# Kernel tuning notes

Measured on AMD Instinct MI355X. Metric: run time of the kernel, lower is better.

The kernel has to match this reference:

```python
import jax, jax.numpy as jnp
import numpy as np

B, C, H, W = 4, 256, 64, 64

def _conv1x1(x, w, b):
    # x: [B,C,H,W], w: [O,C] (1x1 conv kernel squeezed), b: [O]
    return jnp.einsum('bchw,oc->bohw', x, w) + b[None, :, None, None]

def setup_inputs() -> dict:
    key = jax.random.key(0)
    ks = jax.random.split(key, 9)
    s = 1.0 / np.sqrt(C)
    inp = {'x': jax.random.normal(ks[0], (B, C, H, W), dtype=jnp.float32)}
    for i, name in enumerate(['f', 'g', 'h', 'v']):
        inp['W' + name] = jax.random.uniform(ks[1 + 2 * i], (C, C), jnp.float32, -s, s)
        inp['b' + name] = jax.random.uniform(ks[2 + 2 * i], (C,), jnp.float32, -s, s)
    return inp

def reference(x, Wf, bf, Wg, bg, Wh, bh, Wv, bv):
    b, c, h, w = x.shape
    n = h * w
    f = _conv1x1(x, Wf, bf).reshape(b, c, n)  # [B,C,N]
    g = _conv1x1(x, Wg, bg).reshape(b, c, n)  # [B,C,N]
    hh = _conv1x1(x, Wh, bh).reshape(b, c, n)  # [B,C,N]
    fg = jnp.einsum('bci,bcj->bij', f, g)      # [B,N,N], no scaling (as in source)
    attn = jax.nn.softmax(fg, axis=1)          # softmax over dim=1 (first N axis)
    fgh = jnp.einsum('bci,bij->bcj', hh, attn) # [B,C,N]
    return _conv1x1(fgh.reshape(b, c, h, w), Wv, bv)
```

## Files before the change

### kernel.cpp

```cpp
#include <hip/hip_runtime.h>
#include <hip/hip_bf16.h>


typedef short short8 __attribute__((ext_vector_type(8)));
typedef short short4v __attribute__((ext_vector_type(4)));
typedef float f32x4 __attribute__((ext_vector_type(4)));
typedef _Float16 f16x8 __attribute__((ext_vector_type(8)));
typedef unsigned short u16;
typedef unsigned int u32;

#define DEV static __device__ __forceinline__
#define MFMA16(a, b, c) __builtin_amdgcn_mfma_f32_16x16x32_f16(a, b, c, 0, 0, 0)

DEV u16 h16(float x) {
    union { _Float16 h; u16 u; } c;
    c.h = (_Float16)x;
    return c.u;
}
DEV f16x8 ldh8(const u16* p) { return *reinterpret_cast<const f16x8*>(p); }

DEV u32 cvtpk(float a, float b) {
    u32 r;
    asm("v_cvt_pkrtz_f16_f32 %0, %1, %2" : "=v"(r) : "v"(a), "v"(b));
    return r;
}

DEV void gload16(const void* g, void* l) {
    __builtin_amdgcn_global_load_lds(
        (const __attribute__((address_space(1))) unsigned int*)g,
        (__attribute__((address_space(3))) unsigned int*)l, 16, 0, 0);
}

constexpr size_t OFF_WH = 0;
constexpr size_t OFF_WV = 131072;
constexpr size_t OFF_MB = 262144;
constexpr size_t OFF_ML = 266240;
constexpr size_t OFF_M  = 524288;
constexpr size_t OFF_U  = 1310720;
constexpr size_t OFF_H  = OFF_U + 8388608;
constexpr size_t OFF_XT = OFF_H + 8388608;
constexpr size_t OFF_OP = OFF_XT + 8388608;

__global__ __launch_bounds__(256) void k_prep_w(
    const float* __restrict__ Wh, const float* __restrict__ Wv, u16* WH, u16* WV) {
    int i = blockIdx.x * 256 + threadIdx.x;
    WH[i] = h16(Wh[i]);
    WV[i] = h16(Wv[i]);
}

__global__ __launch_bounds__(256) void k_gemm_M(
    const float* __restrict__ Wf, const float* __restrict__ Wg,
    const float* __restrict__ bg, u16* __restrict__ M, float* __restrict__ Mb) {
    int c = blockIdx.x;
    int t = threadIdx.x;
    __shared__ float wf[256];
    wf[t] = Wf[(size_t)t * 256 + c];
    __syncthreads();
    float acc = 0.f;
    for (int o = 0; o < 256; ++o) acc += wf[o] * Wg[(size_t)o * 256 + t];
    M[(size_t)c * 256 + t] = h16(acc);
    if (t == 0) {
        float s = 0.f;
        for (int o = 0; o < 256; ++o) s += wf[o] * bg[o];
        Mb[c] = s;
    }
}

__global__ __launch_bounds__(256) void k_prep_x(const float* __restrict__ x, u16* Xt) {
    __shared__ float lds[64][65];
    int bid = blockIdx.x;
    int b = bid >> 8, rem = bid & 255, ct = rem >> 6, nt = rem & 63;
    int tid = threadIdx.x;
    int tx = tid & 63, ty = tid >> 6;
    const float* src = x + ((size_t)(b * 256 + ct * 64)) * 4096 + nt * 64;
#pragma unroll
    for (int k = 0; k < 16; ++k) {
        int cl = ty * 16 + k;
        lds[cl][tx] = src[(size_t)cl * 4096 + tx];
    }
    __syncthreads();
    int nl = tid >> 2, cg = tid & 3;
    short8 h0, h1;
#pragma unroll
    for (int j = 0; j < 8; ++j) h0[j] = (short)h16(lds[cg * 16 + j][nl]);
#pragma unroll
    for (int j = 8; j < 16; ++j) h1[j - 8] = (short)h16(lds[cg * 16 + j][nl]);
    size_t dst = ((size_t)(b * 4096 + nt * 64 + nl)) * 256 + ct * 64 + cg * 16;
    *reinterpret_cast<short8*>(Xt + dst) = h0;
    *reinterpret_cast<short8*>(Xt + dst + 8) = h1;
}

__global__ __launch_bounds__(256) void k_conv_u(
    const u16* __restrict__ Xt, const u16* __restrict__ M,
    const float* __restrict__ Mb, u16* U) {
    int bidm = blockIdx.x & 255, bido = blockIdx.x >> 8;
    int w = threadIdx.x >> 6, lane = threadIdx.x & 63, r = lane & 15, g = lane >> 4;
    int m0 = bidm * 64 + w * 16, o0 = bido * 64;
    f32x4 ua[4];
#pragma unroll
    for (int i = 0; i < 4; ++i) ua[i] = {0.f, 0.f, 0.f, 0.f};
    const u16* ar = Xt + (size_t)(m0 + r) * 256;
#pragma unroll
    for (int ks = 0; ks < 8; ++ks) {
        int k0 = ks * 32 + 8 * g;
        f16x8 a = ldh8(ar + k0);
#pragma unroll
        for (int ot = 0; ot < 4; ++ot) {
            size_t wrow = (size_t)(o0 + ot * 16 + r) * 256 + k0;
            ua[ot] = MFMA16(a, ldh8(M + wrow), ua[ot]);
        }
    }
#pragma unroll
    for (int ot = 0; ot < 4; ++ot) {
#pragma unroll
        for (int q = 0; q < 4; ++q) {
            int row = m0 + 4 * g + q;
            int col = o0 + ot * 16 + r;
            U[(size_t)row * 256 + col] = h16(ua[ot][q] + Mb[col]);
        }
    }
}

__global__ __launch_bounds__(256) void k_conv_h(
    const u16* __restrict__ WH, const u16* __restrict__ Xt,
    const float* __restrict__ bh, u16* Hb) {
    int bidn = blockIdx.x & 255, bido = blockIdx.x >> 8;
    int w = threadIdx.x >> 6, lane = threadIdx.x & 63, r = lane & 15, g = lane >> 4;
    int o0 = bido * 64 + w * 16, n0 = bidn * 64;
    f32x4 acc[4];
#pragma unroll
    for (int i = 0; i < 4; ++i) acc[i] = {0.f, 0.f, 0.f, 0.f};
    const u16* arow = WH + (size_t)(o0 + r) * 256;
#pragma unroll
    for (int ks = 0; ks < 8; ++ks) {
        int k0 = ks * 32 + 8 * g;
        f16x8 a = ldh8(arow + k0);
#pragma unroll
        for (int ntl = 0; ntl < 4; ++ntl) {
            f16x8 bb = ldh8(Xt + (size_t)(n0 + ntl * 16 + r) * 256 + k0);
            acc[ntl] = MFMA16(a, bb, acc[ntl]);
        }
    }
#pragma unroll
    for (int ntl = 0; ntl < 4; ++ntl) {
#pragma unroll
        for (int q = 0; q < 4; ++q) {
            int o = o0 + 4 * g + q;
            int nf = n0 + ntl * 16 + r;
            int bb = nf >> 12, n = nf & 4095;
            int k5 = n & 31;
            int kp = (k5 < 16) ? (8 * (k5 >> 2) + (k5 & 3))
                               : (8 * ((k5 - 16) >> 2) + 4 + (k5 & 3));
            int np = (n & ~31) | kp;
            Hb[((size_t)(bb * 256 + o)) * 4096 + np] = h16(acc[ntl][q] + bh[o]);
        }
    }
}

__global__ __launch_bounds__(256, 2) void k_attn(
    const u16* __restrict__ F, const u16* __restrict__ G,
    const u16* __restrict__ Hb, u16* __restrict__ OP, float* __restrict__ ML) {
    __shared__ u16 Kd[2][8192];
    __shared__ u16 Vd[2][8192];

    int bid = blockIdx.x;
    int xcd = bid & 7, idx = bid >> 3;
    int b = xcd >> 1, ks = xcd & 1;
    int tid = threadIdx.x;
    int w = tid >> 6, lane = tid & 63, r = lane & 15, g = lane >> 4;
    int j0 = idx * 64 + w * 16;
    const float L2E = 1.4426950408889634f;

    int vlc = (r >> 1) * 128 + (((16 * g) + (r & 1) * 64) ^ (((r >> 1) & 7) << 4));

    f16x8 Qf[8];
    {
        const u16* q = G + (size_t)(b * 4096 + j0 + r) * 256;
#pragma unroll
        for (int k = 0; k < 8; ++k) Qf[k] = ldh8(q + k * 32 + 8 * g);
    }
    f32x4 O[16];
#pragma unroll
    for (int i = 0; i < 16; ++i) O[i] = {0.f, 0.f, 0.f, 0.f};
    float m = -1e30f, l = 0.f;

    const char* Fb  = (const char*)(F + (size_t)b * 4096 * 256);
    const char* Hbb = (const char*)(Hb + (size_t)b * 256 * 4096);

    int ksrc[4], vsrc[4];
#pragma unroll
    for (int t = 0; t < 4; ++t) {
        int d = (w * 4 + t) * 1024 + lane * 16;
        int row = d >> 9, col = d & 511;
        ksrc[t] = row * 512 + (col ^ ((row & 7) << 4));
        int r128 = d >> 7, wn = d & 127;
        int wp = wn ^ ((r128 & 7) << 4);
        vsrc[t] = ((r128 * 2 + (wp >> 6)) << 13) + (wp & 63);
    }

#define STAGE(bufn, I0)                                                         \
    do {                                                                        \
        const char* kb_ = Fb + (size_t)(I0) * 512;                              \
        const char* vb_ = Hbb + (size_t)(I0) * 2;                               \
        char* kl = (char*)Kd[bufn];                                             \
        char* vl = (char*)Vd[bufn];                                             \
        _Pragma("unroll") for (int t = 0; t < 4; ++t)                           \
            gload16(kb_ + ksrc[t], kl + (w * 4 + t) * 1024);                    \
        _Pragma("unroll") for (int t = 0; t < 4; ++t)                           \
            gload16(vb_ + vsrc[t], vl + (w * 4 + t) * 1024);                    \
    } while (0)

    int i0beg = ks * 2048;
    STAGE(0, i0beg);
    __syncthreads();

    for (int it = 0; it < 64; ++it) {
        int cur = it & 1;
        if (it + 1 < 64) STAGE(cur ^ 1, i0beg + (it + 1) * 32);

        const char* Kl = (const char*)Kd[cur];
        const char* Vb = (const char*)Vd[cur] + vlc;

        f32x4 s0 = {0.f, 0.f, 0.f, 0.f};
        f32x4 s1 = {0.f, 0.f, 0.f, 0.f};
        __builtin_amdgcn_s_setprio(1);
        {
            const char* kr = Kl + r * 512;
            int sw = (r & 7) << 4;
#pragma unroll
            for (int k = 0; k < 8; ++k) {
                f16x8 ka = *reinterpret_cast<const f16x8*>(kr + ((k * 64 + 16 * g) ^ sw));
                s0 = MFMA16(ka, Qf[k], s0);
            }
        }
        {
            const char* kr = Kl + (16 + r) * 512;
            int sw = (r & 7) << 4;
#pragma unroll
            for (int k = 0; k < 8; ++k) {
                f16x8 ka = *reinterpret_cast<const f16x8*>(kr + ((k * 64 + 16 * g) ^ sw));
                s1 = MFMA16(ka, Qf[k], s1);
            }
        }
        __builtin_amdgcn_s_setprio(0);

        float v = fmaxf(fmaxf(fmaxf(s0[0], s0[1]), fmaxf(s0[2], s0[3])),
                        fmaxf(fmaxf(s1[0], s1[1]), fmaxf(s1[2], s1[3])));
        if (!__all(v - m <= 8.0f)) {
            v = fmaxf(v, __shfl_xor(v, 16));
            v = fmaxf(v, __shfl_xor(v, 32));
            float mn = fmaxf(m, v);
            float corr = exp2f((m - mn) * L2E);
            m = mn;
            l *= corr;
#pragma unroll
            for (int ct = 0; ct < 16; ++ct) O[ct] *= corr;
        }
#pragma unroll
        for (int q = 0; q < 4; ++q) {
            s0[q] = exp2f((s0[q] - m) * L2E);
            s1[q] = exp2f((s1[q] - m) * L2E);
        }
        l += (s0[0] + s0[1] + s0[2] + s0[3]) + (s1[0] + s1[1] + s1[2] + s1[3]);

        union { u32 wd[4]; f16x8 fr; } pu;
        pu.wd[0] = cvtpk(s0[0], s0[1]);
        pu.wd[1] = cvtpk(s0[2], s0[3]);
        pu.wd[2] = cvtpk(s1[0], s1[1]);
        pu.wd[3] = cvtpk(s1[2], s1[3]);

        __builtin_amdgcn_s_setprio(1);
#pragma unroll
        for (int ct = 0; ct < 16; ++ct) {
            f16x8 vb = *reinterpret_cast<const f16x8*>(Vb + ct * 1024);
            O[ct] = MFMA16(vb, pu.fr, O[ct]);
        }
        __builtin_amdgcn_s_setprio(0);

        __syncthreads();
    }
#undef STAGE

    l += __shfl_xor(l, 16);
    l += __shfl_xor(l, 32);
    float inv = 1.f / l;
    size_t mrow = (size_t)ks * 16384 + b * 4096 + j0 + r;
#pragma unroll
    for (int ct = 0; ct < 16; ++ct) {
        short4v pk;
#pragma unroll
        for (int q = 0; q < 4; ++q) pk[q] = (short)h16(O[ct][q] * inv);
        *reinterpret_cast<short4v*>(OP + mrow * 256 + ct * 16 + 4 * g) = pk;
    }
    if (g == 0) {
        size_t mi = mrow * 2;
        ML[mi] = m;
        ML[mi + 1] = l;
    }
}

__global__ __launch_bounds__(256) void k_conv_out(
    const u16* __restrict__ WV, const u16* __restrict__ OP,
    const float* __restrict__ ML, const float* __restrict__ bv,
    float* __restrict__ out) {
    int bidn = blockIdx.x & 255, bido = blockIdx.x >> 8;
    int w = threadIdx.x >> 6, lane = threadIdx.x & 63, r = lane & 15, g = lane >> 4;
    int o0 = bido * 64 + w * 16, n0 = bidn * 64;
    const float L2E = 1.4426950408889634f;
    float wl0[4], wl1[4];
    int nfs[4];
#pragma unroll
    for (int ntl = 0; ntl < 4; ++ntl) {
        int nf = n0 + ntl * 16 + r;
        nfs[ntl] = nf;
        float m0_ = ML[(size_t)nf * 2], l0_ = ML[(size_t)nf * 2 + 1];
        float m1_ = ML[((size_t)16384 + nf) * 2], l1_ = ML[((size_t)16384 + nf) * 2 + 1];
        float M_ = fmaxf(m0_, m1_);
        float a0 = exp2f((m0_ - M_) * L2E) * l0_;
        float a1 = exp2f((m1_ - M_) * L2E) * l1_;
        float inv = 1.f / (a0 + a1);
        wl0[ntl] = a0 * inv;
        wl1[ntl] = a1 * inv;
    }
    f32x4 acc[4];
#pragma unroll
    for (int i = 0; i < 4; ++i) acc[i] = {0.f, 0.f, 0.f, 0.f};
    const u16* arow = WV + (size_t)(o0 + r) * 256;
#pragma unroll
    for (int ks = 0; ks < 8; ++ks) {
        int k0 = ks * 32 + 8 * g;
        f16x8 a = ldh8(arow + k0);
#pragma unroll
        for (int ntl = 0; ntl < 4; ++ntl) {
            f16x8 v0 = ldh8(OP + (size_t)nfs[ntl] * 256 + k0);
            f16x8 v1 = ldh8(OP + ((size_t)16384 + nfs[ntl]) * 256 + k0);
            union { u32 wd[4]; f16x8 fr; } bb;
#pragma unroll
            for (int j = 0; j < 4; ++j) {
                float e0 = wl0[ntl] * (float)v0[2 * j] + wl1[ntl] * (float)v1[2 * j];
                float e1 = wl0[ntl] * (float)v0[2 * j + 1] + wl1[ntl] * (float)v1[2 * j + 1];
                bb.wd[j] = cvtpk(e0, e1);
            }
            acc[ntl] = MFMA16(a, bb.fr, acc[ntl]);
        }
    }
#pragma unroll
    for (int ntl = 0; ntl < 4; ++ntl) {
#pragma unroll
        for (int q = 0; q < 4; ++q) {
            int o = o0 + 4 * g + q;
            int nf = nfs[ntl];
            int bb2 = nf >> 12, n = nf & 4095;
            out[((size_t)(bb2 * 256 + o)) * 4096 + n] = acc[ntl][q] + bv[o];
        }
    }
}

extern "C" void kernel_launch(void* const* d_in, const int* in_sizes, int n_in,
                              void* d_out, int out_size, void* d_ws, size_t ws_size,
                              hipStream_t stream) {
    const float* x  = (const float*)d_in[0];
    const float* Wf = (const float*)d_in[1];
    const float* bf = (const float*)d_in[2];
    const float* Wg = (const float*)d_in[3];
    const float* bg = (const float*)d_in[4];
    const float* Wh = (const float*)d_in[5];
    const float* bh = (const float*)d_in[6];
    const float* Wv = (const float*)d_in[7];
    const float* bv = (const float*)d_in[8];
    float* out = (float*)d_out;
    char* ws = (char*)d_ws;
    (void)bf;

    u16* WH = (u16*)(ws + OFF_WH);
    u16* WV = (u16*)(ws + OFF_WV);
    float* MB = (float*)(ws + OFF_MB);
    float* ML = (float*)(ws + OFF_ML);
    u16* M  = (u16*)(ws + OFF_M);
    u16* U  = (u16*)(ws + OFF_U);
    u16* H  = (u16*)(ws + OFF_H);
    u16* XT = (u16*)(ws + OFF_XT);
    u16* OP = (u16*)(ws + OFF_OP);

    k_prep_w<<<256, 256, 0, stream>>>(Wh, Wv, WH, WV);
    k_gemm_M<<<256, 256, 0, stream>>>(Wf, Wg, bg, M, MB);
    k_prep_x<<<1024, 256, 0, stream>>>(x, XT);
    k_conv_u<<<1024, 256, 0, stream>>>(XT, M, MB, U);
    k_conv_h<<<1024, 256, 0, stream>>>(WH, XT, bh, H);
    k_attn<<<512, 256, 0, stream>>>(XT, U, H, OP, ML);
    k_conv_out<<<1024, 256, 0, stream>>>(WV, OP, ML, bv, out);
}
```

Before: 211.4 us.

## Fuse x transpose with U and H projections; fold weight cast into M kernel

The fp16 weight conversion moves into the M-product kernel. The x transpose, the U projection and the H projection merge into one kernel that keeps a 64-row x tile in LDS and reuses it for both GEMMs. This removes three launches and the re-reads of Xt from global memory. The cost is that the fused kernel runs only 256 blocks and each block loops serially over all 256 output channels, so parallelism is lower.

```diff
diff --git a/kernel.cpp b/kernel.cpp
--- a/kernel.cpp
+++ b/kernel.cpp
@@ -41,24 +41,22 @@
 constexpr size_t OFF_XT = OFF_H + 8388608;
 constexpr size_t OFF_OP = OFF_XT + 8388608;
 
-__global__ __launch_bounds__(256) void k_prep_w(
-    const float* __restrict__ Wh, const float* __restrict__ Wv, u16* WH, u16* WV) {
-    int i = blockIdx.x * 256 + threadIdx.x;
-    WH[i] = h16(Wh[i]);
-    WV[i] = h16(Wv[i]);
-}
-
 __global__ __launch_bounds__(256) void k_gemm_M(
     const float* __restrict__ Wf, const float* __restrict__ Wg,
-    const float* __restrict__ bg, u16* __restrict__ M, float* __restrict__ Mb) {
+    const float* __restrict__ bg, const float* __restrict__ Wh,
+    const float* __restrict__ Wv,
+    u16* __restrict__ M, float* __restrict__ Mb, u16* WH, u16* WV) {
     int c = blockIdx.x;
     int t = threadIdx.x;
+    size_t rowi = (size_t)c * 256 + t;
+    WH[rowi] = h16(Wh[rowi]);
+    WV[rowi] = h16(Wv[rowi]);
     __shared__ float wf[256];
     wf[t] = Wf[(size_t)t * 256 + c];
     __syncthreads();
     float acc = 0.f;
     for (int o = 0; o < 256; ++o) acc += wf[o] * Wg[(size_t)o * 256 + t];
-    M[(size_t)c * 256 + t] = h16(acc);
+    M[rowi] = h16(acc);
     if (t == 0) {
         float s = 0.f;
         for (int o = 0; o < 256; ++o) s += wf[o] * bg[o];
@@ -66,93 +64,74 @@
     }
 }
 
-__global__ __launch_bounds__(256) void k_prep_x(const float* __restrict__ x, u16* Xt) {
-    __shared__ float lds[64][65];
+__global__ __launch_bounds__(256) void k_prep(
+    const float* __restrict__ x, const u16* __restrict__ M,
+    const float* __restrict__ Mb, const u16* __restrict__ WH,
+    const float* __restrict__ bh,
+    u16* __restrict__ Xt, u16* __restrict__ U, u16* __restrict__ Hb) {
+    __shared__ float tbuf[64][65];
+    __shared__ u16 xt[64][264];
+
     int bid = blockIdx.x;
-    int b = bid >> 8, rem = bid & 255, ct = rem >> 6, nt = rem & 63;
+    int m0 = bid * 64;
+    int b = m0 >> 12, n0 = m0 & 4095;
     int tid = threadIdx.x;
     int tx = tid & 63, ty = tid >> 6;
-    const float* src = x + ((size_t)(b * 256 + ct * 64)) * 4096 + nt * 64;
-#pragma unroll
-    for (int k = 0; k < 16; ++k) {
-        int cl = ty * 16 + k;
-        lds[cl][tx] = src[(size_t)cl * 4096 + tx];
-    }
-    __syncthreads();
     int nl = tid >> 2, cg = tid & 3;
-    short8 h0, h1;
-#pragma unroll
-    for (int j = 0; j < 8; ++j) h0[j] = (short)h16(lds[cg * 16 + j][nl]);
-#pragma unroll
-    for (int j = 8; j < 16; ++j) h1[j - 8] = (short)h16(lds[cg * 16 + j][nl]);
-    size_t dst = ((size_t)(b * 4096 + nt * 64 + nl)) * 256 + ct * 64 + cg * 16;
-    *reinterpret_cast<short8*>(Xt + dst) = h0;
-    *reinterpret_cast<short8*>(Xt + dst + 8) = h1;
-}
-
-__global__ __launch_bounds__(256) void k_conv_u(
-    const u16* __restrict__ Xt, const u16* __restrict__ M,
-    const float* __restrict__ Mb, u16* U) {
-    int bidm = blockIdx.x & 255, bido = blockIdx.x >> 8;
-    int w = threadIdx.x >> 6, lane = threadIdx.x & 63, r = lane & 15, g = lane >> 4;
-    int m0 = bidm * 64 + w * 16, o0 = bido * 64;
-    f32x4 ua[4];
-#pragma unroll
-    for (int i = 0; i < 4; ++i) ua[i] = {0.f, 0.f, 0.f, 0.f};
-    const u16* ar = Xt + (size_t)(m0 + r) * 256;
-#pragma unroll
-    for (int ks = 0; ks < 8; ++ks) {
-        int k0 = ks * 32 + 8 * g;
-        f16x8 a = ldh8(ar + k0);
-#pragma unroll
-        for (int ot = 0; ot < 4; ++ot) {
-            size_t wrow = (size_t)(o0 + ot * 16 + r) * 256 + k0;
-            ua[ot] = MFMA16(a, ldh8(M + wrow), ua[ot]);
-        }
-    }
-#pragma unroll
-    for (int ot = 0; ot < 4; ++ot) {
+
+    for (int ct4 = 0; ct4 < 4; ++ct4) {
+        const float* src = x + ((size_t)(b * 256 + ct4 * 64)) * 4096 + n0;
+#pragma unroll
+        for (int k = 0; k < 16; ++k) {
+            int cl = ty * 16 + k;
+            tbuf[cl][tx] = src[(size_t)cl * 4096 + tx];
+        }
+        __syncthreads();
+        short8 h0, h1;
+#pragma unroll
+        for (int j = 0; j < 8; ++j) h0[j] = (short)h16(tbuf[cg * 16 + j][nl]);
+#pragma unroll
+        for (int j = 8; j < 16; ++j) h1[j - 8] = (short)h16(tbuf[cg * 16 + j][nl]);
+        int colbase = ct4 * 64 + cg * 16;
+        *reinterpret_cast<short8*>(&xt[nl][colbase]) = h0;
+        *reinterpret_cast<short8*>(&xt[nl][colbase + 8]) = h1;
+        size_t dst = ((size_t)(m0 + nl)) * 256 + colbase;
+        *reinterpret_cast<short8*>(Xt + dst) = h0;
+        *reinterpret_cast<short8*>(Xt + dst + 8) = h1;
+        __syncthreads();
+    }
+
+    int w = tid >> 6, lane = tid & 63, r = lane & 15, g = lane >> 4;
+    f16x8 A[8];
+#pragma unroll
+    for (int ks = 0; ks < 8; ++ks)
+        A[ks] = *reinterpret_cast<const f16x8*>(&xt[w * 16 + r][ks * 32 + 8 * g]);
+
+#pragma unroll 4
+    for (int ot = 0; ot < 16; ++ot) {
+        f32x4 au = {0.f, 0.f, 0.f, 0.f};
+        f32x4 ah = {0.f, 0.f, 0.f, 0.f};
+        const u16* mrow = M + (size_t)(ot * 16 + r) * 256;
+        const u16* hrow = WH + (size_t)(ot * 16 + r) * 256;
+#pragma unroll
+        for (int ks = 0; ks < 8; ++ks) {
+            int k0 = ks * 32 + 8 * g;
+            au = MFMA16(A[ks], ldh8(mrow + k0), au);
+            ah = MFMA16(A[ks], ldh8(hrow + k0), ah);
+        }
+        int o = ot * 16 + r;
+        float mb = Mb[o];
+        float bhv = bh[o];
 #pragma unroll
         for (int q = 0; q < 4; ++q) {
-            int row = m0 + 4 * g + q;
-            int col = o0 + ot * 16 + r;
-            U[(size_t)row * 256 + col] = h16(ua[ot][q] + Mb[col]);
-        }
-    }
-}
-
-__global__ __launch_bounds__(256) void k_conv_h(
-    const u16* __restrict__ WH, const u16* __restrict__ Xt,
-    const float* __restrict__ bh, u16* Hb) {
-    int bidn = blockIdx.x & 255, bido = blockIdx.x >> 8;
-    int w = threadIdx.x >> 6, lane = threadIdx.x & 63, r = lane & 15, g = lane >> 4;
-    int o0 = bido * 64 + w * 16, n0 = bidn * 64;
-    f32x4 acc[4];
-#pragma unroll
-    for (int i = 0; i < 4; ++i) acc[i] = {0.f, 0.f, 0.f, 0.f};
-    const u16* arow = WH + (size_t)(o0 + r) * 256;
-#pragma unroll
-    for (int ks = 0; ks < 8; ++ks) {
-        int k0 = ks * 32 + 8 * g;
-        f16x8 a = ldh8(arow + k0);
-#pragma unroll
-        for (int ntl = 0; ntl < 4; ++ntl) {
-            f16x8 bb = ldh8(Xt + (size_t)(n0 + ntl * 16 + r) * 256 + k0);
-            acc[ntl] = MFMA16(a, bb, acc[ntl]);
-        }
-    }
-#pragma unroll
-    for (int ntl = 0; ntl < 4; ++ntl) {
-#pragma unroll
-        for (int q = 0; q < 4; ++q) {
-            int o = o0 + 4 * g + q;
-            int nf = n0 + ntl * 16 + r;
-            int bb = nf >> 12, n = nf & 4095;
+            int rloc = w * 16 + 4 * g + q;
+            U[(size_t)(m0 + rloc) * 256 + o] = h16(au[q] + mb);
+            int n = n0 + rloc;
             int k5 = n & 31;
             int kp = (k5 < 16) ? (8 * (k5 >> 2) + (k5 & 3))
                                : (8 * ((k5 - 16) >> 2) + 4 + (k5 & 3));
             int np = (n & ~31) | kp;
-            Hb[((size_t)(bb * 256 + o)) * 4096 + np] = h16(acc[ntl][q] + bh[o]);
+            Hb[((size_t)(b * 256 + o)) * 4096 + np] = h16(ah[q] + bhv);
         }
     }
 }
@@ -382,11 +361,8 @@
     u16* XT = (u16*)(ws + OFF_XT);
     u16* OP = (u16*)(ws + OFF_OP);
 
-    k_prep_w<<<256, 256, 0, stream>>>(Wh, Wv, WH, WV);
-    k_gemm_M<<<256, 256, 0, stream>>>(Wf, Wg, bg, M, MB);
-    k_prep_x<<<1024, 256, 0, stream>>>(x, XT);
-    k_conv_u<<<1024, 256, 0, stream>>>(XT, M, MB, U);
-    k_conv_h<<<1024, 256, 0, stream>>>(WH, XT, bh, H);
+    k_gemm_M<<<256, 256, 0, stream>>>(Wf, Wg, bg, Wh, Wv, M, MB, WH, WV);
+    k_prep<<<256, 256, 0, stream>>>(x, M, MB, WH, bh, XT, U, H);
     k_attn<<<512, 256, 0, stream>>>(XT, U, H, OP, ML);
     k_conv_out<<<1024, 256, 0, stream>>>(WV, OP, ML, bv, out);
 }
```

New measurement: 204.5 us, median of 2. 1.03x faster.
